# Kernel tuning notes

Hardware: AMD Instinct MI355X
Metric: run time of the kernel (lower is better)

The kernel has to match this reference:

```python
import jax, jax.numpy as jnp
import numpy as np

GROUPS = 32
N_HEADS = 8
EPS = 1e-5


def setup_inputs() -> dict:
    key = jax.random.key(0)
    ks = jax.random.split(key, 4)
    B, C, H, W = 8, 512, 32, 32
    x = jax.random.normal(ks[0], (B, C, H, W), dtype=jnp.float32)
    norm_scale = jnp.ones((C,), jnp.float32)
    norm_bias = jnp.zeros((C,), jnp.float32)
    qkv_w = jax.random.normal(ks[1], (3 * C, C), jnp.float32) * (C ** -0.5)
    qkv_b = jnp.zeros((3 * C,), jnp.float32)
    proj_w = jax.random.normal(ks[2], (C, C), jnp.float32) * (C ** -0.5)
    proj_b = jnp.zeros((C,), jnp.float32)
    return {"x": x, "norm_scale": norm_scale, "norm_bias": norm_bias,
            "qkv_w": qkv_w, "qkv_b": qkv_b, "proj_w": proj_w, "proj_b": proj_b}


def reference(x, norm_scale, norm_bias, qkv_w, qkv_b, proj_w, proj_b):
    B, C, H, W = x.shape
    T = H * W
    xf = x.reshape(B, C, T)

    # GroupNorm32 (32 groups, computed in float32, affine)
    xg = xf.astype(jnp.float32).reshape(B, GROUPS, C // GROUPS, T)
    mean = xg.mean(axis=(2, 3), keepdims=True)
    var = xg.var(axis=(2, 3), keepdims=True)
    xn = ((xg - mean) * jax.lax.rsqrt(var + EPS)).reshape(B, C, T)
    xn = (xn * norm_scale[:, None] + norm_bias[:, None]).astype(x.dtype)

    # qkv: 1x1 conv1d == pointwise matmul -> [B, 3C, T]
    qkv = jnp.einsum('oc,bct->bot', qkv_w, xn) + qkv_b[:, None]

    # QKVAttentionLegacy: reshape to [B*H, 3*ch, T], split
    ch = C // N_HEADS
    qkv_h = qkv.reshape(B * N_HEADS, 3 * ch, T)
    q, k, v = qkv_h[:, :ch], qkv_h[:, ch:2 * ch], qkv_h[:, 2 * ch:]
    scale = ch ** -0.25
    weight = jnp.einsum('bct,bcs->bts', q * scale, k * scale)  # [B*H, T, T]
    weight = jax.nn.softmax(weight.astype(jnp.float32), axis=-1).astype(qkv.dtype)
    a = jnp.einsum('bts,bcs->bct', weight, v).reshape(B, C, T)

    # proj_out (1x1 conv) + residual
    h = jnp.einsum('oc,bct->bot', proj_w, a) + proj_b[:, None]
    return (xf + h).reshape(B, C, H, W)
```

## Files before the change

kernel.cpp:

```cpp
#include <hip/hip_runtime.h>
#include <hip/hip_bf16.h>
#include <stdint.h>

typedef unsigned short u16;
typedef unsigned int u32;
typedef __bf16 bf16x8 __attribute__((ext_vector_type(8)));
typedef float f32x4 __attribute__((ext_vector_type(4)));


static __device__ __forceinline__ u16 f2bf(float f) {
  union { __hip_bfloat16 h; u16 u; } c;
  c.h = __float2bfloat16(f);
  return c.u;
}

static __device__ __forceinline__ void gload_lds16(const void* g, void* l) {
  __builtin_amdgcn_global_load_lds(
      (__attribute__((address_space(1))) u32*)(uintptr_t)g,
      (__attribute__((address_space(3))) u32*)l, 16, 0, 0);
}

__global__ __launch_bounds__(256) void wcvt(const float* __restrict__ wq,
                                            const float* __restrict__ wp,
                                            u16* __restrict__ wqb,
                                            u16* __restrict__ wpb) {
  int idx = (blockIdx.x * 256 + threadIdx.x) * 4;
  const float* s;
  u16* d;
  if (idx < 786432) { s = wq + idx; d = wqb + idx; }
  else { int k = idx - 786432; s = wp + k; d = wpb + k; }
  float4 v = *(const float4*)s;
  uint2 o;
  o.x = (u32)f2bf(v.x) | ((u32)f2bf(v.y) << 16);
  o.y = (u32)f2bf(v.z) | ((u32)f2bf(v.w) << 16);
  *(uint2*)d = o;
}

__global__ __launch_bounds__(256) void gn_stats(const float* __restrict__ x,
                                                float* __restrict__ st) {
  int bg = blockIdx.x;
  const float* p = x + (size_t)bg * 16384;
  float s1 = 0.f, s2 = 0.f;
  for (int i = threadIdx.x * 4; i < 16384; i += 1024) {
    float4 v = *(const float4*)(p + i);
    s1 += v.x + v.y + v.z + v.w;
    s2 += v.x * v.x + v.y * v.y + v.z * v.z + v.w * v.w;
  }
#pragma unroll
  for (int off = 1; off < 64; off <<= 1) {
    s1 += __shfl_xor(s1, off);
    s2 += __shfl_xor(s2, off);
  }
  __shared__ float r1[4], r2[4];
  int w = threadIdx.x >> 6, l = threadIdx.x & 63;
  if (l == 0) { r1[w] = s1; r2[w] = s2; }
  __syncthreads();
  if (threadIdx.x == 0) {
    float t1 = r1[0] + r1[1] + r1[2] + r1[3];
    float t2 = r2[0] + r2[1] + r2[2] + r2[3];
    float mean = t1 * (1.f / 16384.f);
    float var = t2 * (1.f / 16384.f) - mean * mean;
    st[bg * 2] = mean;
    st[bg * 2 + 1] = rsqrtf(var + 1e-5f);
  }
}

__global__ __launch_bounds__(256) void gn_apply(const float* __restrict__ x,
                                                const float* __restrict__ st,
                                                const float* __restrict__ ns,
                                                const float* __restrict__ nbi,
                                                u16* __restrict__ xnt) {
  __shared__ u16 tile[32 * 520];
  int b = blockIdx.x >> 5;
  int t0 = (blockIdx.x & 31) << 5;
  int tid = threadIdx.x;
  int tl = tid & 31, cg = tid >> 5;
#pragma unroll 4
  for (int cc = 0; cc < 64; ++cc) {
    int c = cc * 8 + cg;
    float mean = st[(b * 32 + (c >> 4)) * 2];
    float rstd = st[(b * 32 + (c >> 4)) * 2 + 1];
    float v = x[(size_t)b * 524288 + (size_t)c * 1024 + t0 + tl];
    float vn = (v - mean) * rstd * ns[c] + nbi[c];
    tile[tl * 520 + c] = f2bf(vn);
  }
  __syncthreads();
#pragma unroll
  for (int i = 0; i < 8; ++i) {
    int chunk = i * 256 + tid;
    int tl2 = chunk >> 6;
    int c0 = (chunk & 63) * 8;
    uint4 d = *(const uint4*)(tile + tl2 * 520 + c0);
    *(uint4*)(xnt + (size_t)b * 524288 + (size_t)(t0 + tl2) * 512 + c0) = d;
  }
}

static __device__ __forceinline__ void gemm_core(const u16* Abase, const u16* Bbase,
                                                 f32x4 acc[4][4], u16* As, u16* Bs,
                                                 int w, int l, int wm, int wn) {
  const int r8 = l >> 3, ch = l & 7;
  const int fr = l & 15, fq = l >> 4;
#pragma unroll 1
  for (int kt = 0; kt < 8; ++kt) {
    __syncthreads();
#pragma unroll
    for (int i = 0; i < 4; ++i) {
      int gi = (w << 2) + i;
      int row = (gi << 3) + r8;
      int xoff = ((ch ^ (row & 7)) << 4);
      gload_lds16((const char*)Abase + (size_t)row * 1024 + (kt << 7) + xoff,
                  (char*)As + (gi << 10));
      gload_lds16((const char*)Bbase + (size_t)row * 1024 + (kt << 7) + xoff,
                  (char*)Bs + (gi << 10));
    }
    __syncthreads();
#pragma unroll
    for (int kf = 0; kf < 2; ++kf) {
      bf16x8 af[4], bfv[4];
#pragma unroll
      for (int i = 0; i < 4; ++i) {
        int rowA = wm * 64 + i * 16 + fr;
        af[i] = *(const bf16x8*)(As + rowA * 64 + ((((kf << 2) + fq) ^ (rowA & 7)) << 3));
        int rowB = wn * 64 + i * 16 + fr;
        bfv[i] = *(const bf16x8*)(Bs + rowB * 64 + ((((kf << 2) + fq) ^ (rowB & 7)) << 3));
      }
#pragma unroll
      for (int i = 0; i < 4; ++i)
#pragma unroll
        for (int j = 0; j < 4; ++j)
          acc[i][j] = __builtin_amdgcn_mfma_f32_16x16x32_bf16(af[i], bfv[j], acc[i][j], 0, 0, 0);
    }
  }
}

__global__ __launch_bounds__(256) void gemm_qkv(const u16* __restrict__ Wq,
                                                const u16* __restrict__ Xnt,
                                                const float* __restrict__ bq,
                                                u16* __restrict__ qT,
                                                u16* __restrict__ kT,
                                                u16* __restrict__ vv) {
  __shared__ u16 As[128 * 64];
  __shared__ u16 Bs[128 * 64];
  int bid = blockIdx.x;
  int mb = bid % 12, nb = (bid / 12) % 8, b = bid / 96;
  int tid = threadIdx.x, w = tid >> 6, l = tid & 63;
  int wm = w >> 1, wn = w & 1;
  f32x4 acc[4][4];
#pragma unroll
  for (int i = 0; i < 4; ++i)
#pragma unroll
    for (int j = 0; j < 4; ++j) acc[i][j] = (f32x4){0.f, 0.f, 0.f, 0.f};

  gemm_core(Wq + (size_t)mb * 65536, Xnt + (size_t)b * 524288 + (size_t)nb * 65536,
            acc, As, Bs, w, l, wm, wn);

  int fr = l & 15, fq = l >> 4;
#pragma unroll
  for (int i = 0; i < 4; ++i) {
    int o0 = mb * 128 + wm * 64 + i * 16 + fq * 4;
    int h = o0 / 192, j0 = o0 % 192;
    int seg = j0 >> 6, off = j0 & 63;
    float qksc = (seg == 0) ? 0.51011687f : 0.35355339f;
    float b0 = bq[o0], b1 = bq[o0 + 1], b2 = bq[o0 + 2], b3 = bq[o0 + 3];
    size_t hb = (size_t)(b * 8 + h) * 65536;
#pragma unroll
    for (int j = 0; j < 4; ++j) {
      int t = nb * 128 + wn * 64 + j * 16 + fr;
      f32x4 v = acc[i][j];
      if (seg < 2) {
        u16* dst = (seg == 0 ? qT : kT) + hb + (size_t)t * 64 + off;
        uint2 pk;
        pk.x = (u32)f2bf((v[0] + b0) * qksc) | ((u32)f2bf((v[1] + b1) * qksc) << 16);
        pk.y = (u32)f2bf((v[2] + b2) * qksc) | ((u32)f2bf((v[3] + b3) * qksc) << 16);
        *(uint2*)dst = pk;
      } else {
        u16* dst = vv + hb + (size_t)off * 1024 + t;
        dst[0] = f2bf(v[0] + b0);
        dst[1024] = f2bf(v[1] + b1);
        dst[2048] = f2bf(v[2] + b2);
        dst[3072] = f2bf(v[3] + b3);
      }
    }
  }
}

__global__ __launch_bounds__(256) void attn(const u16* __restrict__ qT,
                                            const u16* __restrict__ kT,
                                            const u16* __restrict__ vv,
                                            u16* __restrict__ aT) {
  __shared__ u16 Ks[64 * 64];
  __shared__ u16 Vs[80 * 64];
  __shared__ u16 Ps[4 * 16 * 72];
  int bid = blockIdx.x;
  int bh = (bid & 7) * 8 + (bid >> 7);
  int tq = (bid >> 3) & 15;
  int tid = threadIdx.x, w = tid >> 6, l = tid & 63;
  int fr = l & 15, fq = l >> 4;
  int r8 = l >> 3, ch = l & 7;
  size_t hb = (size_t)bh * 65536;

  {
    int row = 64 + (tid >> 4);
    int c4 = (tid & 15) * 4;
    u16 val = (row == 64) ? (u16)0x3F80 : (u16)0;
    u16* p = Vs + row * 64 + c4;
    p[0] = val; p[1] = val; p[2] = val; p[3] = val;
  }

  bf16x8 aq[2];
  {
    const u16* qp = qT + hb + (size_t)(tq * 64 + w * 16 + fr) * 64 + fq * 8;
    aq[0] = *(const bf16x8*)(qp);
    aq[1] = *(const bf16x8*)(qp + 32);
  }

  f32x4 acc_o[4];
  f32x4 acc_s = (f32x4){0.f, 0.f, 0.f, 0.f};
#pragma unroll
  for (int nb = 0; nb < 4; ++nb) acc_o[nb] = (f32x4){0.f, 0.f, 0.f, 0.f};

  u16* pw = Ps + w * (16 * 72);

  for (int st = 0; st < 16; ++st) {
    __syncthreads();
#pragma unroll
    for (int i = 0; i < 2; ++i) {
      int gi = (w << 1) + i;
      int row = (gi << 3) + r8;
      int xoff = ((ch ^ (row & 7)) << 4);
      gload_lds16((const char*)(kT + hb) + (size_t)(st * 64 + row) * 128 + xoff,
                  (char*)Ks + (gi << 10));
      gload_lds16((const char*)(vv + hb) + (size_t)row * 2048 + st * 128 + xoff,
                  (char*)Vs + (gi << 10));
    }
    __syncthreads();

    f32x4 sa[4];
#pragma unroll
    for (int nb = 0; nb < 4; ++nb) sa[nb] = (f32x4){0.f, 0.f, 0.f, 0.f};
    __builtin_amdgcn_s_setprio(1);
#pragma unroll
    for (int nb = 0; nb < 4; ++nb) {
      int krow = nb * 16 + fr;
#pragma unroll
      for (int kf = 0; kf < 2; ++kf) {
        bf16x8 bk = *(const bf16x8*)(Ks + krow * 64 + ((((kf << 2) + fq) ^ (krow & 7)) << 3));
        sa[nb] = __builtin_amdgcn_mfma_f32_16x16x32_bf16(aq[kf], bk, sa[nb], 0, 0, 0);
      }
    }
    __builtin_amdgcn_s_setprio(0);

#pragma unroll
    for (int nb = 0; nb < 4; ++nb)
#pragma unroll
      for (int r = 0; r < 4; ++r)
        pw[(fq * 4 + r) * 72 + nb * 16 + fr] = f2bf(exp2f(sa[nb][r]));

    bf16x8 ap[2];
#pragma unroll
    for (int kf = 0; kf < 2; ++kf)
      ap[kf] = *(const bf16x8*)(pw + fr * 72 + kf * 32 + fq * 8);

    __builtin_amdgcn_s_setprio(1);
#pragma unroll
    for (int nb = 0; nb < 4; ++nb) {
      int vrow = nb * 16 + fr;
#pragma unroll
      for (int kf = 0; kf < 2; ++kf) {
        bf16x8 bv = *(const bf16x8*)(Vs + vrow * 64 + ((((kf << 2) + fq) ^ (vrow & 7)) << 3));
        acc_o[nb] = __builtin_amdgcn_mfma_f32_16x16x32_bf16(ap[kf], bv, acc_o[nb], 0, 0, 0);
      }
    }
    {
      int vrow = 64 + fr;
#pragma unroll
      for (int kf = 0; kf < 2; ++kf) {
        bf16x8 bv = *(const bf16x8*)(Vs + vrow * 64 + ((((kf << 2) + fq) ^ (vrow & 7)) << 3));
        acc_s = __builtin_amdgcn_mfma_f32_16x16x32_bf16(ap[kf], bv, acc_s, 0, 0, 0);
      }
    }
    __builtin_amdgcn_s_setprio(0);
  }

  int b = bh >> 3, h = bh & 7;
  f32x4 invl;
#pragma unroll
  for (int r = 0; r < 4; ++r) invl[r] = 1.f / __shfl(acc_s[r], l & 48);
#pragma unroll
  for (int nb = 0; nb < 4; ++nb) {
    f32x4 ov = acc_o[nb] * invl;
#pragma unroll
    for (int r = 0; r < 4; ++r) {
      int t = tq * 64 + w * 16 + fq * 4 + r;
      aT[(size_t)b * 524288 + (size_t)t * 512 + h * 64 + nb * 16 + fr] = f2bf(ov[r]);
    }
  }
}

__global__ __launch_bounds__(256) void gemm_proj(const u16* __restrict__ Wp,
                                                 const u16* __restrict__ aT,
                                                 const float* __restrict__ bp,
                                                 const float* __restrict__ x,
                                                 float* __restrict__ out) {
  __shared__ u16 As[128 * 64];
  __shared__ u16 Bs[128 * 64];
  int bid = blockIdx.x;
  int mb = bid & 3, nb = (bid >> 2) & 7, b = bid >> 5;
  int tid = threadIdx.x, w = tid >> 6, l = tid & 63;
  int wm = w >> 1, wn = w & 1;
  f32x4 acc[4][4];
#pragma unroll
  for (int i = 0; i < 4; ++i)
#pragma unroll
    for (int j = 0; j < 4; ++j) acc[i][j] = (f32x4){0.f, 0.f, 0.f, 0.f};

  gemm_core(Wp + (size_t)mb * 65536, aT + (size_t)b * 524288 + (size_t)nb * 65536,
            acc, As, Bs, w, l, wm, wn);

  int fr = l & 15, fq = l >> 4;
#pragma unroll
  for (int i = 0; i < 4; ++i) {
    int o0 = mb * 128 + wm * 64 + i * 16 + fq * 4;
    float b0 = bp[o0], b1 = bp[o0 + 1], b2 = bp[o0 + 2], b3 = bp[o0 + 3];
#pragma unroll
    for (int j = 0; j < 4; ++j) {
      int t = nb * 128 + wn * 64 + j * 16 + fr;
      f32x4 v = acc[i][j];
      size_t base = (size_t)b * 524288 + (size_t)o0 * 1024 + t;
      out[base] = x[base] + v[0] + b0;
      out[base + 1024] = x[base + 1024] + v[1] + b1;
      out[base + 2048] = x[base + 2048] + v[2] + b2;
      out[base + 3072] = x[base + 3072] + v[3] + b3;
    }
  }
}

extern "C" void kernel_launch(void* const* d_in, const int* in_sizes, int n_in,
                              void* d_out, int out_size, void* d_ws, size_t ws_size,
                              hipStream_t stream) {
  const float* x = (const float*)d_in[0];
  const float* ns = (const float*)d_in[1];
  const float* nbi = (const float*)d_in[2];
  const float* wq = (const float*)d_in[3];
  const float* bq = (const float*)d_in[4];
  const float* wp = (const float*)d_in[5];
  const float* bp = (const float*)d_in[6];
  float* out = (float*)d_out;
  char* ws = (char*)d_ws;

  u16* wqb = (u16*)(ws);
  u16* wpb = (u16*)(ws + 1572864);
  float* st = (float*)(ws + 2097152);
  u16* xnt = (u16*)(ws + 2101248);
  u16* qT = (u16*)(ws + 2101248 + 8388608);
  u16* kT = (u16*)(ws + 2101248 + 2 * 8388608);
  u16* vv = (u16*)(ws + 2101248 + 3 * 8388608);
  u16* aT = xnt;

  hipLaunchKernelGGL(wcvt, dim3(1024), dim3(256), 0, stream, wq, wp, wqb, wpb);
  hipLaunchKernelGGL(gn_stats, dim3(256), dim3(256), 0, stream, x, st);
  hipLaunchKernelGGL(gn_apply, dim3(256), dim3(256), 0, stream, x, st, ns, nbi, xnt);
  hipLaunchKernelGGL(gemm_qkv, dim3(768), dim3(256), 0, stream, wqb, xnt, bq, qT, kT, vv);
  hipLaunchKernelGGL(attn, dim3(1024), dim3(256), 0, stream, qT, kT, vv, aT);
  hipLaunchKernelGGL(gemm_proj, dim3(256), dim3(256), 0, stream, wpb, aT, bp, x, out);
}
```

Before: 105.4 us.

## Double-buffer LDS tiles in GEMM and attention loops to overlap loads

Converts the GEMM core and the attention K/V loop to double-buffered LDS staging. The next tile's global-to-LDS loads are issued before computing on the current tile, and each iteration needs one barrier instead of two. The goal is to hide global load latency behind MFMA work, at the cost of twice the LDS per block, which may lower occupancy. The buffer offsets are reworked for the larger arrays, and the ones-row in V is written into both buffers.

```diff
diff --git a/kernel.cpp b/kernel.cpp
--- a/kernel.cpp
+++ b/kernel.cpp
@@ -100,29 +100,31 @@
                                                  int w, int l, int wm, int wn) {
   const int r8 = l >> 3, ch = l & 7;
   const int fr = l & 15, fq = l >> 4;
-#pragma unroll 1
-  for (int kt = 0; kt < 8; ++kt) {
-    __syncthreads();
+
+  auto STAGE = [&](int buf, int kt) {
 #pragma unroll
     for (int i = 0; i < 4; ++i) {
       int gi = (w << 2) + i;
       int row = (gi << 3) + r8;
       int xoff = ((ch ^ (row & 7)) << 4);
       gload_lds16((const char*)Abase + (size_t)row * 1024 + (kt << 7) + xoff,
-                  (char*)As + (gi << 10));
+                  (char*)As + (buf << 14) + (gi << 10));
       gload_lds16((const char*)Bbase + (size_t)row * 1024 + (kt << 7) + xoff,
-                  (char*)Bs + (gi << 10));
-    }
-    __syncthreads();
+                  (char*)Bs + (buf << 14) + (gi << 10));
+    }
+  };
+  auto COMPUTE = [&](int buf) {
+    const u16* Ab = As + (buf << 13);
+    const u16* Bb = Bs + (buf << 13);
 #pragma unroll
     for (int kf = 0; kf < 2; ++kf) {
       bf16x8 af[4], bfv[4];
 #pragma unroll
       for (int i = 0; i < 4; ++i) {
         int rowA = wm * 64 + i * 16 + fr;
-        af[i] = *(const bf16x8*)(As + rowA * 64 + ((((kf << 2) + fq) ^ (rowA & 7)) << 3));
+        af[i] = *(const bf16x8*)(Ab + rowA * 64 + ((((kf << 2) + fq) ^ (rowA & 7)) << 3));
         int rowB = wn * 64 + i * 16 + fr;
-        bfv[i] = *(const bf16x8*)(Bs + rowB * 64 + ((((kf << 2) + fq) ^ (rowB & 7)) << 3));
+        bfv[i] = *(const bf16x8*)(Bb + rowB * 64 + ((((kf << 2) + fq) ^ (rowB & 7)) << 3));
       }
 #pragma unroll
       for (int i = 0; i < 4; ++i)
@@ -130,7 +132,19 @@
         for (int j = 0; j < 4; ++j)
           acc[i][j] = __builtin_amdgcn_mfma_f32_16x16x32_bf16(af[i], bfv[j], acc[i][j], 0, 0, 0);
     }
-  }
+  };
+
+  STAGE(0, 0);
+  __syncthreads();
+  int cur = 0;
+#pragma unroll 1
+  for (int kt = 0; kt < 7; ++kt) {
+    STAGE(cur ^ 1, kt + 1);
+    COMPUTE(cur);
+    __syncthreads();
+    cur ^= 1;
+  }
+  COMPUTE(cur);
 }
 
 __global__ __launch_bounds__(256) void gemm_qkv(const u16* __restrict__ Wq,
@@ -139,8 +153,8 @@
                                                 u16* __restrict__ qT,
                                                 u16* __restrict__ kT,
                                                 u16* __restrict__ vv) {
-  __shared__ u16 As[128 * 64];
-  __shared__ u16 Bs[128 * 64];
+  __shared__ u16 As[2 * 128 * 64];
+  __shared__ u16 Bs[2 * 128 * 64];
   int bid = blockIdx.x;
   int mb = bid % 12, nb = (bid / 12) % 8, b = bid / 96;
   int tid = threadIdx.x, w = tid >> 6, l = tid & 63;
@@ -188,8 +202,8 @@
                                             const u16* __restrict__ kT,
                                             const u16* __restrict__ vv,
                                             u16* __restrict__ aT) {
-  __shared__ u16 Ks[64 * 64];
-  __shared__ u16 Vs[80 * 64];
+  __shared__ u16 Ks[2 * 64 * 64];
+  __shared__ u16 Vs[2 * 80 * 64];
   __shared__ u16 Ps[4 * 16 * 72];
   int bid = blockIdx.x;
   int bh = (bid & 7) * 8 + (bid >> 7);
@@ -203,8 +217,11 @@
     int row = 64 + (tid >> 4);
     int c4 = (tid & 15) * 4;
     u16 val = (row == 64) ? (u16)0x3F80 : (u16)0;
-    u16* p = Vs + row * 64 + c4;
-    p[0] = val; p[1] = val; p[2] = val; p[3] = val;
+#pragma unroll
+    for (int bfi = 0; bfi < 2; ++bfi) {
+      u16* p = Vs + bfi * 5120 + row * 64 + c4;
+      p[0] = val; p[1] = val; p[2] = val; p[3] = val;
+    }
   }
 
   bf16x8 aq[2];
@@ -214,26 +231,35 @@
     aq[1] = *(const bf16x8*)(qp + 32);
   }
 
-  f32x4 acc_o[4];
-  f32x4 acc_s = (f32x4){0.f, 0.f, 0.f, 0.f};
-#pragma unroll
-  for (int nb = 0; nb < 4; ++nb) acc_o[nb] = (f32x4){0.f, 0.f, 0.f, 0.f};
-
-  u16* pw = Ps + w * (16 * 72);
-
-  for (int st = 0; st < 16; ++st) {
-    __syncthreads();
+  auto STAGE = [&](int buf, int st) {
 #pragma unroll
     for (int i = 0; i < 2; ++i) {
       int gi = (w << 1) + i;
       int row = (gi << 3) + r8;
       int xoff = ((ch ^ (row & 7)) << 4);
       gload_lds16((const char*)(kT + hb) + (size_t)(st * 64 + row) * 128 + xoff,
-                  (char*)Ks + (gi << 10));
+                  (char*)Ks + (buf << 13) + (gi << 10));
       gload_lds16((const char*)(vv + hb) + (size_t)row * 2048 + st * 128 + xoff,
-                  (char*)Vs + (gi << 10));
-    }
-    __syncthreads();
+                  (char*)Vs + buf * 10240 + (gi << 10));
+    }
+  };
+
+  f32x4 acc_o[4];
+  f32x4 acc_s = (f32x4){0.f, 0.f, 0.f, 0.f};
+#pragma unroll
+  for (int nb = 0; nb < 4; ++nb) acc_o[nb] = (f32x4){0.f, 0.f, 0.f, 0.f};
+
+  u16* pw = Ps + w * (16 * 72);
+
+  STAGE(0, 0);
+  __syncthreads();
+  int cur = 0;
+
+#pragma unroll 1
+  for (int st = 0; st < 16; ++st) {
+    if (st < 15) STAGE(cur ^ 1, st + 1);
+    const u16* Kb = Ks + (cur << 12);
+    const u16* Vb = Vs + cur * 5120;
 
     f32x4 sa[4];
 #pragma unroll
@@ -244,7 +270,7 @@
       int krow = nb * 16 + fr;
 #pragma unroll
       for (int kf = 0; kf < 2; ++kf) {
-        bf16x8 bk = *(const bf16x8*)(Ks + krow * 64 + ((((kf << 2) + fq) ^ (krow & 7)) << 3));
+        bf16x8 bk = *(const bf16x8*)(Kb + krow * 64 + ((((kf << 2) + fq) ^ (krow & 7)) << 3));
         sa[nb] = __builtin_amdgcn_mfma_f32_16x16x32_bf16(aq[kf], bk, sa[nb], 0, 0, 0);
       }
     }
@@ -267,7 +293,7 @@
       int vrow = nb * 16 + fr;
 #pragma unroll
       for (int kf = 0; kf < 2; ++kf) {
-        bf16x8 bv = *(const bf16x8*)(Vs + vrow * 64 + ((((kf << 2) + fq) ^ (vrow & 7)) << 3));
+        bf16x8 bv = *(const bf16x8*)(Vb + vrow * 64 + ((((kf << 2) + fq) ^ (vrow & 7)) << 3));
         acc_o[nb] = __builtin_amdgcn_mfma_f32_16x16x32_bf16(ap[kf], bv, acc_o[nb], 0, 0, 0);
       }
     }
@@ -275,11 +301,14 @@
       int vrow = 64 + fr;
 #pragma unroll
       for (int kf = 0; kf < 2; ++kf) {
-        bf16x8 bv = *(const bf16x8*)(Vs + vrow * 64 + ((((kf << 2) + fq) ^ (vrow & 7)) << 3));
+        bf16x8 bv = *(const bf16x8*)(Vb + vrow * 64 + ((((kf << 2) + fq) ^ (vrow & 7)) << 3));
         acc_s = __builtin_amdgcn_mfma_f32_16x16x32_bf16(ap[kf], bv, acc_s, 0, 0, 0);
       }
     }
     __builtin_amdgcn_s_setprio(0);
+
+    __syncthreads();
+    cur ^= 1;
   }
 
   int b = bh >> 3, h = bh & 7;
@@ -302,8 +331,8 @@
                                                  const float* __restrict__ bp,
                                                  const float* __restrict__ x,
                                                  float* __restrict__ out) {
-  __shared__ u16 As[128 * 64];
-  __shared__ u16 Bs[128 * 64];
+  __shared__ u16 As[2 * 128 * 64];
+  __shared__ u16 Bs[2 * 128 * 64];
   int bid = blockIdx.x;
   int mb = bid & 3, nb = (bid >> 2) & 7, b = bid >> 5;
   int tid = threadIdx.x, w = tid >> 6, l = tid & 63;
```

After: 113.6 us. +7.7%, slower.
